# Kernel tuning notes

Measured on AMD Instinct MI355X. Metric: run time of the kernel, lower is better.

## Reference

```python
import jax, jax.numpy as jnp
import numpy as np

NUM_HEADS = 4
NUM_GROUPS = 32
EPS = 1e-5


def group_norm(x, gamma, beta):
    B, C, H, W = x.shape
    g = x.reshape(B, NUM_GROUPS, C // NUM_GROUPS, H, W)
    mean = g.mean(axis=(2, 3, 4), keepdims=True)
    var = g.var(axis=(2, 3, 4), keepdims=True)
    g = (g - mean) * jax.lax.rsqrt(var + EPS)
    x = g.reshape(B, C, H, W)
    return x * gamma[None, :, None, None] + beta[None, :, None, None]


def setup_inputs() -> dict:
    key = jax.random.key(0)
    ks = jax.random.split(key, 7)
    B, C, H, W = 16, 256, 32, 32
    x = jax.random.normal(ks[0], (B, C, H, W), dtype=jnp.float32)
    gn_gamma = jnp.ones((C,), dtype=jnp.float32)
    gn_beta = jnp.zeros((C,), dtype=jnp.float32)
    s = 1.0 / np.sqrt(C)
    qkv_w = jax.random.normal(ks[1], (3 * C, C), dtype=jnp.float32) * s
    qkv_b = jnp.zeros((3 * C,), dtype=jnp.float32)
    proj_w = jax.random.normal(ks[2], (C, C), dtype=jnp.float32) * s
    proj_b = jnp.zeros((C,), dtype=jnp.float32)
    return {"x": x, "gn_gamma": gn_gamma, "gn_beta": gn_beta,
            "qkv_w": qkv_w, "qkv_b": qkv_b, "proj_w": proj_w, "proj_b": proj_b}


def reference(x, gn_gamma, gn_beta, qkv_w, qkv_b, proj_w, proj_b):
    B, C, H, W = x.shape
    nh = NUM_HEADS
    d = C // nh
    N = H * W

    h = group_norm(x, gn_gamma, gn_beta)
    # 1x1 conv == channel matmul
    qkv = jnp.einsum('bchw,oc->bohw', h, qkv_w) + qkv_b[None, :, None, None]
    qkv = qkv.reshape(B, 3, nh, d, N)
    q, k, v = qkv[:, 0], qkv[:, 1], qkv[:, 2]  # each [B, nh, d, N]

    scale = 1.0 / jnp.sqrt(jnp.asarray(d, dtype=x.dtype))
    attn = jnp.einsum('bhdn,bhdm->bhnm', q, k) * scale  # [B, nh, N, N]
    attn = jax.nn.softmax(attn, axis=-1)
    out = jnp.einsum('bhnm,bhdm->bhdn', attn, v)  # [B, nh, d, N]
    out = out.reshape(B, C, H, W)

    out = jnp.einsum('bchw,oc->bohw', out, proj_w) + proj_b[None, :, None, None]
    return x + out
```

## Files before the change

kernel.cpp:

```cpp
#include <hip/hip_runtime.h>
#include <math.h>

typedef unsigned short u16;
typedef unsigned int u32;
typedef __attribute__((ext_vector_type(8))) short s16x8;
typedef __attribute__((ext_vector_type(4))) float f32x4;

#define NB 16
#define NN 1024
#define GN_EPS 1e-5f

static __device__ __forceinline__ u16 f2bf(float f) {
    union { float f; u32 u; } v; v.f = f;
    return (u16)((v.u + 0x8000u) >> 16);
}
static __device__ __forceinline__ u32 pk2(float a, float b) {
    union { float f; u32 u; } A, B; A.f = a; B.f = b;
    return __builtin_amdgcn_perm(A.u + 0x8000u, B.u + 0x8000u, 0x03020706u);
}

__global__ __launch_bounds__(256) void gn_stats_kernel(
    const float* __restrict__ x, float2* __restrict__ stats)
{
    const int bg = blockIdx.x;
    const int t  = threadIdx.x;
    const size_t base = (size_t)bg * 8192;
    float s = 0.f, ss = 0.f;
#pragma unroll
    for (int i = 0; i < 32; ++i) {
        float v = x[base + t + i * 256];
        s += v; ss += v * v;
    }
#pragma unroll
    for (int off = 32; off > 0; off >>= 1) {
        s  += __shfl_down(s, off);
        ss += __shfl_down(ss, off);
    }
    __shared__ float red[8];
    const int wid = t >> 6;
    if ((t & 63) == 0) { red[wid] = s; red[4 + wid] = ss; }
    __syncthreads();
    if (t == 0) {
        float sa = red[0] + red[1] + red[2] + red[3];
        float sb = red[4] + red[5] + red[6] + red[7];
        float mean = sa * (1.0f / 8192.0f);
        float var  = sb * (1.0f / 8192.0f) - mean * mean;
        stats[bg] = make_float2(mean, 1.0f / sqrtf(var + GN_EPS));
    }
}

__global__ __launch_bounds__(256) void wcvt_kernel(
    const float* __restrict__ qkv_w, const float* __restrict__ proj_w,
    u16* __restrict__ wqb, u16* __restrict__ wpb)
{
    int i = blockIdx.x * 256 + threadIdx.x;
    if (i < 49152) {
        float4 f = ((const float4*)qkv_w)[i];
        *(uint2*)(wqb + (size_t)i * 4) = make_uint2(pk2(f.x, f.y), pk2(f.z, f.w));
    } else {
        int j = i - 49152;
        float4 f = ((const float4*)proj_w)[j];
        *(uint2*)(wpb + (size_t)j * 4) = make_uint2(pk2(f.x, f.y), pk2(f.z, f.w));
    }
}

__global__ __launch_bounds__(256) void gnorm_t_kernel(
    const float* __restrict__ x, const float2* __restrict__ stats,
    const float* __restrict__ gamma, const float* __restrict__ beta,
    u16* __restrict__ Xt)
{
    const int b = blockIdx.z, ct = blockIdx.y, nt = blockIdx.x;
    const int t = threadIdx.x;
    __shared__ float T[64][65];
    const float* xb = x + ((size_t)b * 256 + ct * 64) * NN + nt * 64;
#pragma unroll
    for (int i = 0; i < 16; ++i) {
        int idx = t + i * 256;
        int cr = idx >> 6, col = idx & 63;
        int ch = ct * 64 + cr;
        float2 st = stats[b * 32 + (ch >> 3)];
        float v = xb[(size_t)cr * NN + col];
        T[cr][col] = (v - st.x) * st.y * gamma[ch] + beta[ch];
    }
    __syncthreads();
    u16* dst = Xt + ((size_t)b * NN + nt * 64) * 256 + ct * 64;
#pragma unroll
    for (int p = 0; p < 2; ++p) {
        int idx = t + p * 256;
        int nl = idx >> 3, c8 = idx & 7;
        s16x8 pv;
#pragma unroll
        for (int j = 0; j < 8; ++j) pv[j] = (short)f2bf(T[c8 * 8 + j][nl]);
        *(s16x8*)(dst + (size_t)nl * 256 + c8 * 8) = pv;
    }
}

__global__ __launch_bounds__(256) void qkv_mfma_kernel(
    const u16* __restrict__ Wb, const float* __restrict__ bias,
    const u16* __restrict__ Xt,
    u16* __restrict__ qh, u16* __restrict__ kh, u16* __restrict__ vh)
{
    const int b = blockIdx.z, ot = blockIdx.y, nt = blockIdx.x;
    const int t = threadIdx.x, w = t >> 6, l = t & 63;
    const int g = l >> 4, c = l & 15;
    __shared__ u16 Xlds[32 * 512];
    __shared__ u16 Wlds[16 * 512];
    const u16* Xb = Xt + ((size_t)b * NN + nt * 128) * 256;
    const u16* Wo = Wb + (size_t)ot * 64 * 256;

    const int part = ot >> 2, h = ot & 3;
    const size_t bhoff = (size_t)(b * 4 + h) << 16;

    if (part < 2) {
        f32x4 acc[2][4];
#pragma unroll
        for (int i = 0; i < 2; ++i)
#pragma unroll
            for (int j = 0; j < 4; ++j) acc[i][j] = (f32x4){0.f, 0.f, 0.f, 0.f};
        for (int kk = 0; kk < 256; kk += 128) {
            if (kk) __syncthreads();
#pragma unroll
            for (int s = w; s < 32; s += 4) {
                int nsub = s >> 2, ks = s & 3;
                s16x8 v = *(const s16x8*)(Xb + (size_t)(nsub * 16 + c) * 256 + kk + ks * 32 + g * 8);
                *(s16x8*)(Xlds + s * 512 + l * 8) = v;
            }
#pragma unroll
            for (int s = w; s < 16; s += 4) {
                int osub = s >> 2, ks = s & 3;
                s16x8 v = *(const s16x8*)(Wo + (size_t)(osub * 16 + c) * 256 + kk + ks * 32 + g * 8);
                *(s16x8*)(Wlds + s * 512 + l * 8) = v;
            }
            __syncthreads();
#pragma unroll
            for (int ks = 0; ks < 4; ++ks) {
                s16x8 a0 = *(const s16x8*)(Xlds + ((2 * w) * 4 + ks) * 512 + l * 8);
                s16x8 a1 = *(const s16x8*)(Xlds + ((2 * w + 1) * 4 + ks) * 512 + l * 8);
#pragma unroll
                for (int j = 0; j < 4; ++j) {
                    s16x8 bf = *(const s16x8*)(Wlds + (j * 4 + ks) * 512 + l * 8);
                    acc[0][j] = __builtin_amdgcn_mfma_f32_16x16x32_bf16(a0, bf, acc[0][j], 0, 0, 0);
                    acc[1][j] = __builtin_amdgcn_mfma_f32_16x16x32_bf16(a1, bf, acc[1][j], 0, 0, 0);
                }
            }
        }
        const float sc = (part == 0) ? 0.125f : 1.0f;
        float bv[4];
#pragma unroll
        for (int j = 0; j < 4; ++j) bv[j] = bias[ot * 64 + j * 16 + c];
        u16* dst = (part == 0 ? qh : kh) + bhoff + (size_t)(nt * 128) * 64;
#pragma unroll
        for (int i = 0; i < 2; ++i)
#pragma unroll
            for (int j = 0; j < 4; ++j)
#pragma unroll
                for (int r = 0; r < 4; ++r) {
                    int n = (2 * w + i) * 16 + g * 4 + r;
                    dst[(size_t)n * 64 + j * 16 + c] = f2bf((acc[i][j][r] + bv[j]) * sc);
                }
    } else {
        f32x4 acc[8];
#pragma unroll
        for (int j = 0; j < 8; ++j) acc[j] = (f32x4){0.f, 0.f, 0.f, 0.f};
        for (int kk = 0; kk < 256; kk += 128) {
            if (kk) __syncthreads();
#pragma unroll
            for (int s = w; s < 32; s += 4) {
                int nsub = s >> 2, ks = s & 3;
                s16x8 v = *(const s16x8*)(Xb + (size_t)(nsub * 16 + c) * 256 + kk + ks * 32 + g * 8);
                *(s16x8*)(Xlds + s * 512 + l * 8) = v;
            }
#pragma unroll
            for (int s = w; s < 16; s += 4) {
                int osub = s >> 2, ks = s & 3;
                s16x8 v = *(const s16x8*)(Wo + (size_t)(osub * 16 + c) * 256 + kk + ks * 32 + g * 8);
                *(s16x8*)(Wlds + s * 512 + l * 8) = v;
            }
            __syncthreads();
#pragma unroll
            for (int ks = 0; ks < 4; ++ks) {
                s16x8 a = *(const s16x8*)(Wlds + (w * 4 + ks) * 512 + l * 8);
#pragma unroll
                for (int j = 0; j < 8; ++j) {
                    s16x8 xf = *(const s16x8*)(Xlds + (j * 4 + ks) * 512 + l * 8);
                    acc[j] = __builtin_amdgcn_mfma_f32_16x16x32_bf16(a, xf, acc[j], 0, 0, 0);
                }
            }
        }
        float bv[4];
#pragma unroll
        for (int r = 0; r < 4; ++r) bv[r] = bias[ot * 64 + w * 16 + g * 4 + r];
        u16* dst = vh + bhoff;
#pragma unroll
        for (int j = 0; j < 8; ++j)
#pragma unroll
            for (int r = 0; r < 4; ++r) {
                int d = w * 16 + g * 4 + r;
                int m = nt * 128 + j * 16 + c;
                dst[(size_t)d * NN + m] = f2bf(acc[j][r] + bv[r]);
            }
    }
}

__global__ __launch_bounds__(512) void attn_mfma_kernel(
    const u16* __restrict__ qh, const u16* __restrict__ kh,
    const u16* __restrict__ vh, u16* __restrict__ aoT)
{
    const int t = threadIdx.x;
    const int w = t >> 6, l = t & 63;
    const int g = l >> 4, c = l & 15;
    const int bid = blockIdx.x;
    const int xcd = bid & 7;
    const int idx = bid >> 3;
    const int qt  = idx & 7;
    const int grp = (idx >> 3) * 8 + xcd;
    const int b = grp >> 2, h = grp & 3;
    const size_t bhoff = (size_t)grp << 16;
    const int n_base = qt * 128 + w * 16;

    __shared__ u16 Klds[8 * 512];
    __shared__ u16 Vlds[8 * 512];
    __shared__ u16 Plds[8][2 * 512];

    const u16* qb = qh + bhoff;
    const u16* kb = kh + bhoff;
    const u16* vb = vh + bhoff;

    s16x8 qf[2];
#pragma unroll
    for (int u = 0; u < 2; ++u)
        qf[u] = *(const s16x8*)(qb + (size_t)(n_base + c) * 64 + u * 32 + g * 8);

    f32x4 Oacc[4];
    float m_run = -1e30f, l_run = 0.f;
#pragma unroll
    for (int ds = 0; ds < 4; ++ds) Oacc[ds] = (f32x4){0.f, 0.f, 0.f, 0.f};

    u16* pw = &Plds[w][0];

    for (int mt = 0; mt < 16; ++mt) {
        const int m0 = mt * 64;
        __syncthreads();
        {
            int msub = w >> 1, u = w & 1;
            s16x8 kv = *(const s16x8*)(kb + (size_t)(m0 + msub * 16 + c) * 64 + u * 32 + g * 8);
            *(s16x8*)(Klds + w * 512 + l * 8) = kv;
        }
        {
            int dsub = w >> 1, u = w & 1;
            s16x8 vv = *(const s16x8*)(vb + (size_t)(dsub * 16 + c) * NN + m0 + u * 32 + g * 8);
            *(s16x8*)(Vlds + w * 512 + l * 8) = vv;
        }
        __syncthreads();

        f32x4 S[4];
#pragma unroll
        for (int ms = 0; ms < 4; ++ms) S[ms] = (f32x4){0.f, 0.f, 0.f, 0.f};
#pragma unroll
        for (int ms = 0; ms < 4; ++ms)
#pragma unroll
            for (int u = 0; u < 2; ++u) {
                s16x8 af = *(const s16x8*)(Klds + (ms * 2 + u) * 512 + l * 8);
                S[ms] = __builtin_amdgcn_mfma_f32_16x16x32_bf16(af, qf[u], S[ms], 0, 0, 0);
            }

        s16x8 vf[4][2];
#pragma unroll
        for (int ds = 0; ds < 4; ++ds)
#pragma unroll
            for (int u = 0; u < 2; ++u)
                vf[ds][u] = *(const s16x8*)(Vlds + (ds * 2 + u) * 512 + l * 8);

        float tmax = -1e30f;
#pragma unroll
        for (int ms = 0; ms < 4; ++ms)
#pragma unroll
            for (int r = 0; r < 4; ++r) tmax = fmaxf(tmax, S[ms][r]);
        tmax = fmaxf(tmax, __shfl_xor(tmax, 16));
        tmax = fmaxf(tmax, __shfl_xor(tmax, 32));
        if (!__all(tmax <= m_run + 8.f)) {
            float nm  = fmaxf(m_run, tmax);
            float fac = __expf(m_run - nm);
            m_run = nm;
            l_run *= fac;
#pragma unroll
            for (int ds = 0; ds < 4; ++ds)
#pragma unroll
                for (int r = 0; r < 4; ++r) Oacc[ds][r] *= fac;
        }
        const float mm = m_run;
        float rsum = 0.f;
#pragma unroll
        for (int ms = 0; ms < 4; ++ms)
#pragma unroll
            for (int r = 0; r < 4; ++r) {
                float p = __expf(S[ms][r] - mm);
                S[ms][r] = p;
                rsum += p;
            }
        rsum += __shfl_xor(rsum, 16);
        rsum += __shfl_xor(rsum, 32);
        l_run += rsum;
#pragma unroll
        for (int ms = 0; ms < 4; ++ms) {
            u32 d0 = pk2(S[ms][0], S[ms][1]);
            u32 d1 = pk2(S[ms][2], S[ms][3]);
            int off = (ms >> 1) * 512 + ((ms & 1) * 2 + (g >> 1)) * 128 + c * 8 + (g & 1) * 4;
            *(uint2*)(pw + off) = make_uint2(d0, d1);
        }
        asm volatile("s_waitcnt lgkmcnt(0)" ::: "memory");
#pragma unroll
        for (int u = 0; u < 2; ++u) {
            s16x8 pf = *(const s16x8*)(pw + u * 512 + l * 8);
#pragma unroll
            for (int ds = 0; ds < 4; ++ds)
                Oacc[ds] = __builtin_amdgcn_mfma_f32_16x16x32_bf16(vf[ds][u], pf, Oacc[ds], 0, 0, 0);
        }
    }

    u16* aob = aoT + (size_t)b * NN * 256 + h * 64;
    float inv = 1.0f / l_run;
    const size_t nrow = (size_t)(n_base + c) * 256;
#pragma unroll
    for (int ds = 0; ds < 4; ++ds) {
        u32 lo = pk2(Oacc[ds][0] * inv, Oacc[ds][1] * inv);
        u32 hi = pk2(Oacc[ds][2] * inv, Oacc[ds][3] * inv);
        *(uint2*)(aob + nrow + ds * 16 + g * 4) = make_uint2(lo, hi);
    }
}

__global__ __launch_bounds__(256) void proj_mfma_kernel(
    const u16* __restrict__ Wb, const float* __restrict__ bias,
    const u16* __restrict__ aoT, const float* __restrict__ x,
    float* __restrict__ out)
{
    const int b = blockIdx.z, ot = blockIdx.y, nt = blockIdx.x;
    const int t = threadIdx.x, w = t >> 6, l = t & 63;
    const int g = l >> 4, c = l & 15;
    __shared__ u16 Xlds[32 * 512];
    __shared__ u16 Wlds[16 * 512];
    const u16* Xb = aoT + ((size_t)b * NN + nt * 128) * 256;
    const u16* Wo = Wb + (size_t)ot * 64 * 256;

    f32x4 acc[8];
#pragma unroll
    for (int j = 0; j < 8; ++j) acc[j] = (f32x4){0.f, 0.f, 0.f, 0.f};
    for (int kk = 0; kk < 256; kk += 128) {
        if (kk) __syncthreads();
#pragma unroll
        for (int s = w; s < 32; s += 4) {
            int nsub = s >> 2, ks = s & 3;
            s16x8 v = *(const s16x8*)(Xb + (size_t)(nsub * 16 + c) * 256 + kk + ks * 32 + g * 8);
            *(s16x8*)(Xlds + s * 512 + l * 8) = v;
        }
#pragma unroll
        for (int s = w; s < 16; s += 4) {
            int osub = s >> 2, ks = s & 3;
            s16x8 v = *(const s16x8*)(Wo + (size_t)(osub * 16 + c) * 256 + kk + ks * 32 + g * 8);
            *(s16x8*)(Wlds + s * 512 + l * 8) = v;
        }
        __syncthreads();
#pragma unroll
        for (int ks = 0; ks < 4; ++ks) {
            s16x8 a = *(const s16x8*)(Wlds + (w * 4 + ks) * 512 + l * 8);
#pragma unroll
            for (int j = 0; j < 8; ++j) {
                s16x8 xf = *(const s16x8*)(Xlds + (j * 4 + ks) * 512 + l * 8);
                acc[j] = __builtin_amdgcn_mfma_f32_16x16x32_bf16(a, xf, acc[j], 0, 0, 0);
            }
        }
    }
    float bv[4];
#pragma unroll
    for (int r = 0; r < 4; ++r) bv[r] = bias[ot * 64 + w * 16 + g * 4 + r];
#pragma unroll
    for (int j = 0; j < 8; ++j)
#pragma unroll
        for (int r = 0; r < 4; ++r) {
            int o = ot * 64 + w * 16 + g * 4 + r;
            int n = nt * 128 + j * 16 + c;
            size_t addr = ((size_t)b * 256 + o) * NN + n;
            out[addr] = acc[j][r] + bv[r] + x[addr];
        }
}

extern "C" void kernel_launch(void* const* d_in, const int* in_sizes, int n_in,
                              void* d_out, int out_size, void* d_ws, size_t ws_size,
                              hipStream_t stream)
{
    const float* x      = (const float*)d_in[0];
    const float* gamma  = (const float*)d_in[1];
    const float* beta   = (const float*)d_in[2];
    const float* qkv_w  = (const float*)d_in[3];
    const float* qkv_b  = (const float*)d_in[4];
    const float* proj_w = (const float*)d_in[5];
    const float* proj_b = (const float*)d_in[6];
    float* out = (float*)d_out;

    float* ws = (float*)d_ws;
    float2* stats = (float2*)ws;
    u16* Xt  = (u16*)(ws + 1024);
    u16* wqb = Xt + (size_t)4194304;
    u16* wpb = wqb + (size_t)196608;
    u16* qh  = wpb + (size_t)65536;
    u16* kh  = qh + (size_t)4194304;
    u16* vh  = kh + (size_t)4194304;
    u16* aoT = vh + (size_t)4194304;

    gn_stats_kernel<<<dim3(NB * 32), 256, 0, stream>>>(x, stats);
    wcvt_kernel<<<dim3(256), 256, 0, stream>>>(qkv_w, proj_w, wqb, wpb);
    gnorm_t_kernel<<<dim3(16, 4, NB), 256, 0, stream>>>(x, stats, gamma, beta, Xt);

    qkv_mfma_kernel<<<dim3(8, 12, NB), 256, 0, stream>>>(
        wqb, qkv_b, Xt, qh, kh, vh);

    attn_mfma_kernel<<<dim3(512), 512, 0, stream>>>(qh, kh, vh, aoT);

    proj_mfma_kernel<<<dim3(8, 4, NB), 256, 0, stream>>>(
        wpb, proj_b, aoT, x, out);
}
```

Before: 89.35 us.

## Fuse groupnorm stats and normalize, use direct-to-LDS loads, double-buffer attention K/V

Merges the groupnorm statistics and normalize/transpose kernels into one per-group kernel that keeps the group's data in LDS, so x is read once and one launch is dropped. The QKV and projection GEMMs now stage tiles with global_load_lds and read one operand straight from global memory into registers instead of staging it in LDS. The attention kernel double-buffers its K/V tiles with async LDS loads and explicit waitcnt/barriers, so loading the next tile overlaps compute on the current one. The fused groupnorm runs only 512 blocks and writes strided 16-byte chunks, which may lower occupancy and write efficiency.

```diff
diff --git a/kernel.cpp b/kernel.cpp
--- a/kernel.cpp
+++ b/kernel.cpp
@@ -19,33 +19,66 @@
     return __builtin_amdgcn_perm(A.u + 0x8000u, B.u + 0x8000u, 0x03020706u);
 }
 
-__global__ __launch_bounds__(256) void gn_stats_kernel(
-    const float* __restrict__ x, float2* __restrict__ stats)
-{
-    const int bg = blockIdx.x;
+#define GLL16(gp, lp) __builtin_amdgcn_global_load_lds( \
+    (const __attribute__((address_space(1))) void*)(const void*)(gp), \
+    (__attribute__((address_space(3))) void*)(void*)(lp), 16, 0, 0)
+
+__global__ __launch_bounds__(256) void gn_fused_kernel(
+    const float* __restrict__ x, const float* __restrict__ gamma,
+    const float* __restrict__ beta, u16* __restrict__ Xt)
+{
+    const int gg = blockIdx.x;
+    const int b  = blockIdx.y;
     const int t  = threadIdx.x;
-    const size_t base = (size_t)bg * 8192;
+    __shared__ float T[8 * 1028];
+    __shared__ float sred[8];
+    __shared__ float sstat[2];
+    __shared__ float sgb[16];
+
+    const float4* xb = (const float4*)(x + ((size_t)b * 32 + gg) * 8192);
     float s = 0.f, ss = 0.f;
 #pragma unroll
-    for (int i = 0; i < 32; ++i) {
-        float v = x[base + t + i * 256];
-        s += v; ss += v * v;
-    }
+    for (int i = 0; i < 8; ++i) {
+        float4 f = xb[i * 256 + t];
+        *(float4*)&T[i * 1028 + t * 4] = f;
+        s  += f.x + f.y + f.z + f.w;
+        ss += f.x * f.x + f.y * f.y + f.z * f.z + f.w * f.w;
+    }
+    if (t < 8) { sgb[t] = gamma[gg * 8 + t]; sgb[8 + t] = beta[gg * 8 + t]; }
 #pragma unroll
     for (int off = 32; off > 0; off >>= 1) {
         s  += __shfl_down(s, off);
         ss += __shfl_down(ss, off);
     }
-    __shared__ float red[8];
-    const int wid = t >> 6;
-    if ((t & 63) == 0) { red[wid] = s; red[4 + wid] = ss; }
+    if ((t & 63) == 0) { sred[t >> 6] = s; sred[4 + (t >> 6)] = ss; }
     __syncthreads();
     if (t == 0) {
-        float sa = red[0] + red[1] + red[2] + red[3];
-        float sb = red[4] + red[5] + red[6] + red[7];
+        float sa = sred[0] + sred[1] + sred[2] + sred[3];
+        float sb = sred[4] + sred[5] + sred[6] + sred[7];
         float mean = sa * (1.0f / 8192.0f);
         float var  = sb * (1.0f / 8192.0f) - mean * mean;
-        stats[bg] = make_float2(mean, 1.0f / sqrtf(var + GN_EPS));
+        sstat[0] = mean; sstat[1] = 1.0f / sqrtf(var + GN_EPS);
+    }
+    __syncthreads();
+    const float mean = sstat[0], rstd = sstat[1];
+    float gm[8], bt[8];
+#pragma unroll
+    for (int j = 0; j < 8; ++j) {
+        gm[j] = sgb[j] * rstd;
+        bt[j] = sgb[8 + j] - mean * rstd * sgb[j];
+    }
+    u16* dst = Xt + (size_t)b * NN * 256 + gg * 8;
+#pragma unroll
+    for (int rep = 0; rep < 4; ++rep) {
+        int n = rep * 256 + t;
+        u32 o[4];
+#pragma unroll
+        for (int p = 0; p < 4; ++p) {
+            float v0 = T[(2 * p)     * 1028 + n] * gm[2 * p]     + bt[2 * p];
+            float v1 = T[(2 * p + 1) * 1028 + n] * gm[2 * p + 1] + bt[2 * p + 1];
+            o[p] = pk2(v0, v1);
+        }
+        *(uint4*)(dst + (size_t)n * 256) = make_uint4(o[0], o[1], o[2], o[3]);
     }
 }
 
@@ -64,37 +97,6 @@
     }
 }
 
-__global__ __launch_bounds__(256) void gnorm_t_kernel(
-    const float* __restrict__ x, const float2* __restrict__ stats,
-    const float* __restrict__ gamma, const float* __restrict__ beta,
-    u16* __restrict__ Xt)
-{
-    const int b = blockIdx.z, ct = blockIdx.y, nt = blockIdx.x;
-    const int t = threadIdx.x;
-    __shared__ float T[64][65];
-    const float* xb = x + ((size_t)b * 256 + ct * 64) * NN + nt * 64;
-#pragma unroll
-    for (int i = 0; i < 16; ++i) {
-        int idx = t + i * 256;
-        int cr = idx >> 6, col = idx & 63;
-        int ch = ct * 64 + cr;
-        float2 st = stats[b * 32 + (ch >> 3)];
-        float v = xb[(size_t)cr * NN + col];
-        T[cr][col] = (v - st.x) * st.y * gamma[ch] + beta[ch];
-    }
-    __syncthreads();
-    u16* dst = Xt + ((size_t)b * NN + nt * 64) * 256 + ct * 64;
-#pragma unroll
-    for (int p = 0; p < 2; ++p) {
-        int idx = t + p * 256;
-        int nl = idx >> 3, c8 = idx & 7;
-        s16x8 pv;
-#pragma unroll
-        for (int j = 0; j < 8; ++j) pv[j] = (short)f2bf(T[c8 * 8 + j][nl]);
-        *(s16x8*)(dst + (size_t)nl * 256 + c8 * 8) = pv;
-    }
-}
-
 __global__ __launch_bounds__(256) void qkv_mfma_kernel(
     const u16* __restrict__ Wb, const float* __restrict__ bias,
     const u16* __restrict__ Xt,
@@ -103,47 +105,38 @@
     const int b = blockIdx.z, ot = blockIdx.y, nt = blockIdx.x;
     const int t = threadIdx.x, w = t >> 6, l = t & 63;
     const int g = l >> 4, c = l & 15;
-    __shared__ u16 Xlds[32 * 512];
-    __shared__ u16 Wlds[16 * 512];
+    __shared__ u16 Slds[32 * 512];
     const u16* Xb = Xt + ((size_t)b * NN + nt * 128) * 256;
     const u16* Wo = Wb + (size_t)ot * 64 * 256;
-
     const int part = ot >> 2, h = ot & 3;
     const size_t bhoff = (size_t)(b * 4 + h) << 16;
 
     if (part < 2) {
+#pragma unroll
+        for (int s = w; s < 32; s += 4) {
+            int osub = s >> 3, ks = s & 7;
+            GLL16(Wo + (size_t)(osub * 16 + c) * 256 + ks * 32 + g * 8, Slds + s * 512);
+        }
+        s16x8 a0[8], a1[8];
+#pragma unroll
+        for (int ks = 0; ks < 8; ++ks) {
+            a0[ks] = *(const s16x8*)(Xb + (size_t)((2 * w) * 16 + c) * 256 + ks * 32 + g * 8);
+            a1[ks] = *(const s16x8*)(Xb + (size_t)((2 * w + 1) * 16 + c) * 256 + ks * 32 + g * 8);
+        }
         f32x4 acc[2][4];
 #pragma unroll
         for (int i = 0; i < 2; ++i)
 #pragma unroll
             for (int j = 0; j < 4; ++j) acc[i][j] = (f32x4){0.f, 0.f, 0.f, 0.f};
-        for (int kk = 0; kk < 256; kk += 128) {
-            if (kk) __syncthreads();
-#pragma unroll
-            for (int s = w; s < 32; s += 4) {
-                int nsub = s >> 2, ks = s & 3;
-                s16x8 v = *(const s16x8*)(Xb + (size_t)(nsub * 16 + c) * 256 + kk + ks * 32 + g * 8);
-                *(s16x8*)(Xlds + s * 512 + l * 8) = v;
-            }
-#pragma unroll
-            for (int s = w; s < 16; s += 4) {
-                int osub = s >> 2, ks = s & 3;
-                s16x8 v = *(const s16x8*)(Wo + (size_t)(osub * 16 + c) * 256 + kk + ks * 32 + g * 8);
-                *(s16x8*)(Wlds + s * 512 + l * 8) = v;
-            }
-            __syncthreads();
-#pragma unroll
-            for (int ks = 0; ks < 4; ++ks) {
-                s16x8 a0 = *(const s16x8*)(Xlds + ((2 * w) * 4 + ks) * 512 + l * 8);
-                s16x8 a1 = *(const s16x8*)(Xlds + ((2 * w + 1) * 4 + ks) * 512 + l * 8);
-#pragma unroll
-                for (int j = 0; j < 4; ++j) {
-                    s16x8 bf = *(const s16x8*)(Wlds + (j * 4 + ks) * 512 + l * 8);
-                    acc[0][j] = __builtin_amdgcn_mfma_f32_16x16x32_bf16(a0, bf, acc[0][j], 0, 0, 0);
-                    acc[1][j] = __builtin_amdgcn_mfma_f32_16x16x32_bf16(a1, bf, acc[1][j], 0, 0, 0);
-                }
-            }
-        }
+        __syncthreads();
+#pragma unroll
+        for (int ks = 0; ks < 8; ++ks)
+#pragma unroll
+            for (int j = 0; j < 4; ++j) {
+                s16x8 bf = *(const s16x8*)(Slds + (j * 8 + ks) * 512 + l * 8);
+                acc[0][j] = __builtin_amdgcn_mfma_f32_16x16x32_bf16(a0[ks], bf, acc[0][j], 0, 0, 0);
+                acc[1][j] = __builtin_amdgcn_mfma_f32_16x16x32_bf16(a1[ks], bf, acc[1][j], 0, 0, 0);
+            }
         const float sc = (part == 0) ? 0.125f : 1.0f;
         float bv[4];
 #pragma unroll
@@ -167,22 +160,15 @@
 #pragma unroll
             for (int s = w; s < 32; s += 4) {
                 int nsub = s >> 2, ks = s & 3;
-                s16x8 v = *(const s16x8*)(Xb + (size_t)(nsub * 16 + c) * 256 + kk + ks * 32 + g * 8);
-                *(s16x8*)(Xlds + s * 512 + l * 8) = v;
-            }
-#pragma unroll
-            for (int s = w; s < 16; s += 4) {
-                int osub = s >> 2, ks = s & 3;
-                s16x8 v = *(const s16x8*)(Wo + (size_t)(osub * 16 + c) * 256 + kk + ks * 32 + g * 8);
-                *(s16x8*)(Wlds + s * 512 + l * 8) = v;
+                GLL16(Xb + (size_t)(nsub * 16 + c) * 256 + kk + ks * 32 + g * 8, Slds + s * 512);
             }
             __syncthreads();
 #pragma unroll
             for (int ks = 0; ks < 4; ++ks) {
-                s16x8 a = *(const s16x8*)(Wlds + (w * 4 + ks) * 512 + l * 8);
+                s16x8 a = *(const s16x8*)(Wo + (size_t)(w * 16 + c) * 256 + kk + ks * 32 + g * 8);
 #pragma unroll
                 for (int j = 0; j < 8; ++j) {
-                    s16x8 xf = *(const s16x8*)(Xlds + (j * 4 + ks) * 512 + l * 8);
+                    s16x8 xf = *(const s16x8*)(Slds + (j * 4 + ks) * 512 + l * 8);
                     acc[j] = __builtin_amdgcn_mfma_f32_16x16x32_bf16(a, xf, acc[j], 0, 0, 0);
                 }
             }
@@ -218,14 +204,16 @@
     const size_t bhoff = (size_t)grp << 16;
     const int n_base = qt * 128 + w * 16;
 
-    __shared__ u16 Klds[8 * 512];
-    __shared__ u16 Vlds[8 * 512];
+    __shared__ u16 Klds[2][8 * 512];
+    __shared__ u16 Vlds[2][8 * 512];
     __shared__ u16 Plds[8][2 * 512];
 
     const u16* qb = qh + bhoff;
     const u16* kb = kh + bhoff;
     const u16* vb = vh + bhoff;
 
+    const int msub = w >> 1, uu = w & 1;
+
     s16x8 qf[2];
 #pragma unroll
     for (int u = 0; u < 2; ++u)
@@ -238,20 +226,24 @@
 
     u16* pw = &Plds[w][0];
 
+    GLL16(kb + (size_t)(msub * 16 + c) * 64 + uu * 32 + g * 8, &Klds[0][w * 512]);
+    GLL16(vb + (size_t)(msub * 16 + c) * NN + uu * 32 + g * 8, &Vlds[0][w * 512]);
+
     for (int mt = 0; mt < 16; ++mt) {
-        const int m0 = mt * 64;
-        __syncthreads();
-        {
-            int msub = w >> 1, u = w & 1;
-            s16x8 kv = *(const s16x8*)(kb + (size_t)(m0 + msub * 16 + c) * 64 + u * 32 + g * 8);
-            *(s16x8*)(Klds + w * 512 + l * 8) = kv;
-        }
-        {
-            int dsub = w >> 1, u = w & 1;
-            s16x8 vv = *(const s16x8*)(vb + (size_t)(dsub * 16 + c) * NN + m0 + u * 32 + g * 8);
-            *(s16x8*)(Vlds + w * 512 + l * 8) = vv;
-        }
-        __syncthreads();
+        const int cur = mt & 1;
+        if (mt < 15) {
+            const int m1 = (mt + 1) * 64;
+            GLL16(kb + (size_t)(m1 + msub * 16 + c) * 64 + uu * 32 + g * 8, &Klds[cur ^ 1][w * 512]);
+            GLL16(vb + (size_t)(msub * 16 + c) * NN + m1 + uu * 32 + g * 8, &Vlds[cur ^ 1][w * 512]);
+            asm volatile("s_waitcnt vmcnt(2)" ::: "memory");
+        } else {
+            asm volatile("s_waitcnt vmcnt(0)" ::: "memory");
+        }
+        __builtin_amdgcn_s_barrier();
+        asm volatile("" ::: "memory");
+
+        const u16* Kc = &Klds[cur][0];
+        const u16* Vc = &Vlds[cur][0];
 
         f32x4 S[4];
 #pragma unroll
@@ -260,7 +252,7 @@
         for (int ms = 0; ms < 4; ++ms)
 #pragma unroll
             for (int u = 0; u < 2; ++u) {
-                s16x8 af = *(const s16x8*)(Klds + (ms * 2 + u) * 512 + l * 8);
+                s16x8 af = *(const s16x8*)(Kc + (ms * 2 + u) * 512 + l * 8);
                 S[ms] = __builtin_amdgcn_mfma_f32_16x16x32_bf16(af, qf[u], S[ms], 0, 0, 0);
             }
 
@@ -269,7 +261,7 @@
         for (int ds = 0; ds < 4; ++ds)
 #pragma unroll
             for (int u = 0; u < 2; ++u)
-                vf[ds][u] = *(const s16x8*)(Vlds + (ds * 2 + u) * 512 + l * 8);
+                vf[ds][u] = *(const s16x8*)(Vc + (ds * 2 + u) * 512 + l * 8);
 
         float tmax = -1e30f;
 #pragma unroll
@@ -316,6 +308,8 @@
             for (int ds = 0; ds < 4; ++ds)
                 Oacc[ds] = __builtin_amdgcn_mfma_f32_16x16x32_bf16(vf[ds][u], pf, Oacc[ds], 0, 0, 0);
         }
+        asm volatile("" ::: "memory");
+        __builtin_amdgcn_s_barrier();
     }
 
     u16* aob = aoT + (size_t)b * NN * 256 + h * 64;
@@ -337,8 +331,7 @@
     const int b = blockIdx.z, ot = blockIdx.y, nt = blockIdx.x;
     const int t = threadIdx.x, w = t >> 6, l = t & 63;
     const int g = l >> 4, c = l & 15;
-    __shared__ u16 Xlds[32 * 512];
-    __shared__ u16 Wlds[16 * 512];
+    __shared__ u16 Slds[32 * 512];
     const u16* Xb = aoT + ((size_t)b * NN + nt * 128) * 256;
     const u16* Wo = Wb + (size_t)ot * 64 * 256;
 
@@ -350,22 +343,15 @@
 #pragma unroll
         for (int s = w; s < 32; s += 4) {
             int nsub = s >> 2, ks = s & 3;
-            s16x8 v = *(const s16x8*)(Xb + (size_t)(nsub * 16 + c) * 256 + kk + ks * 32 + g * 8);
-            *(s16x8*)(Xlds + s * 512 + l * 8) = v;
-        }
-#pragma unroll
-        for (int s = w; s < 16; s += 4) {
-            int osub = s >> 2, ks = s & 3;
-            s16x8 v = *(const s16x8*)(Wo + (size_t)(osub * 16 + c) * 256 + kk + ks * 32 + g * 8);
-            *(s16x8*)(Wlds + s * 512 + l * 8) = v;
+            GLL16(Xb + (size_t)(nsub * 16 + c) * 256 + kk + ks * 32 + g * 8, Slds + s * 512);
         }
         __syncthreads();
 #pragma unroll
         for (int ks = 0; ks < 4; ++ks) {
-            s16x8 a = *(const s16x8*)(Wlds + (w * 4 + ks) * 512 + l * 8);
+            s16x8 a = *(const s16x8*)(Wo + (size_t)(w * 16 + c) * 256 + kk + ks * 32 + g * 8);
 #pragma unroll
             for (int j = 0; j < 8; ++j) {
-                s16x8 xf = *(const s16x8*)(Xlds + (j * 4 + ks) * 512 + l * 8);
+                s16x8 xf = *(const s16x8*)(Slds + (j * 4 + ks) * 512 + l * 8);
                 acc[j] = __builtin_amdgcn_mfma_f32_16x16x32_bf16(a, xf, acc[j], 0, 0, 0);
             }
         }
@@ -397,9 +383,7 @@
     const float* proj_b = (const float*)d_in[6];
     float* out = (float*)d_out;
 
-    float* ws = (float*)d_ws;
-    float2* stats = (float2*)ws;
-    u16* Xt  = (u16*)(ws + 1024);
+    u16* Xt  = (u16*)d_ws;
     u16* wqb = Xt + (size_t)4194304;
     u16* wpb = wqb + (size_t)196608;
     u16* qh  = wpb + (size_t)65536;
@@ -407,9 +391,8 @@
     u16* vh  = kh + (size_t)4194304;
     u16* aoT = vh + (size_t)4194304;
 
-    gn_stats_kernel<<<dim3(NB * 32), 256, 0, stream>>>(x, stats);
     wcvt_kernel<<<dim3(256), 256, 0, stream>>>(qkv_w, proj_w, wqb, wpb);
-    gnorm_t_kernel<<<dim3(16, 4, NB), 256, 0, stream>>>(x, stats, gamma, beta, Xt);
+    gn_fused_kernel<<<dim3(32, NB), 256, 0, stream>>>(x, gamma, beta, Xt);
 
     qkv_mfma_kernel<<<dim3(8, 12, NB), 256, 0, stream>>>(
         wqb, qkv_b, Xt, qh, kh, vh);
```

Measured after the change: 92.10 us. +3.1%, slower.
